# Optimization experiments

Hardware: AMD Instinct MI355X
Metric: run time of the kernel (lower is better)

The kernel has to match this reference:

```python
import jax, jax.numpy as jnp
import numpy as np

M = 16384
C = 128
CLS_W = 8        # cls window size (even)
CLS_C = 64       # cls_depth
REG_W = 3        # reg window size (odd)
CLS_T = 1.0      # cls_temperature
REG_T = 1.0      # reg_temperature
PAD = REG_W // 2
W1 = CLS_W + 2 * PAD  # 10


def setup_inputs() -> dict:
    key = jax.random.key(0)
    k0, k1 = jax.random.split(key)
    feature0 = jax.random.normal(k0, (M, CLS_W * CLS_W, C), dtype=jnp.float32)
    feature1 = jax.random.normal(k1, (M, W1 * W1, C), dtype=jnp.float32)
    return {"feature0": feature0, "feature1": feature1}


def _inner_mask_indices():
    mask = np.zeros((W1, W1), dtype=bool)
    mask[PAD:-PAD, PAD:-PAD] = True
    return jnp.asarray(np.flatnonzero(mask.ravel()))


def reference(feature0, feature1):
    m = feature0.shape[0]
    reg_c = C - CLS_C
    cls_f0, reg_f0 = feature0[..., :CLS_C], feature0[..., CLS_C:]
    cls_f1, reg_f1 = feature1[..., :CLS_C], feature1[..., CLS_C:]

    # ---- cls branch: windowed correlation + dual softmax ----
    cls_f1m = cls_f1[:, _inner_mask_indices(), :]  # [m, cls_w^2, cls_c]
    sim = jnp.einsum('mlc,msc->mls', cls_f0, cls_f1m) / CLS_C / CLS_T
    heatmap = jax.nn.softmax(sim, axis=1) * jax.nn.softmax(sim, axis=2)  # [m, 64, 64]

    ww = CLS_W * CLS_W
    idx = jnp.argmax(heatmap.reshape(m, -1), axis=1)
    idxes0 = (idx // ww)[:, None]
    idxes1 = (idx % ww)[:, None]

    # kornia create_meshgrid(normalized=False): last dim is (x, y)
    ys, xs = jnp.meshgrid(jnp.arange(CLS_W, dtype=jnp.float32),
                          jnp.arange(CLS_W, dtype=jnp.float32), indexing='ij')
    biases = (jnp.stack([xs, ys], axis=-1) - CLS_W // 2 + 0.5).reshape(-1, 2)
    biases0 = biases[idxes0[:, 0]]
    biases1 = biases[idxes1[:, 0]]

    # ---- reg branch: gather window around top cls match, softmax expectation ----
    r = jnp.arange(m)
    rf0 = reg_f0[r, idxes0[:, 0]]                     # [m, reg_c]
    reg_sp = reg_f1.reshape(m, W1, W1, reg_c)         # spatial layout, row-major
    i1 = idxes1[:, 0] // CLS_W                        # top-left row of the reg window
    j1 = idxes1[:, 0] % CLS_W
    rows = i1[:, None] + jnp.arange(REG_W)            # [m, 3]
    cols = j1[:, None] + jnp.arange(REG_W)            # [m, 3]
    patch = reg_sp[r[:, None, None], rows[:, :, None], cols[:, None, :], :]  # [m,3,3,reg_c]
    rf1 = patch.reshape(m, REG_W * REG_W, reg_c)

    sim_r = jnp.einsum('mc,mrc->mr', rf0, rf1) / jnp.sqrt(jnp.float32(reg_c)) / REG_T
    hm_r = jax.nn.softmax(sim_r, axis=1).reshape(m, REG_W, REG_W)

    # kornia spatial_expectation2d with normalized coordinates in [-1, 1]
    lin = jnp.linspace(-1.0, 1.0, REG_W)
    gy, gx = jnp.meshgrid(lin, lin, indexing='ij')
    reg_biases = jnp.stack([jnp.sum(hm_r * gx, axis=(1, 2)),
                            jnp.sum(hm_r * gy, axis=(1, 2))], axis=-1)  # [m, 2]

    return heatmap, idxes0, idxes1, biases0, biases1, reg_biases
```

## Files before the change

kernel.cpp:

```cpp
#include <hip/hip_runtime.h>

__device__ __forceinline__ void gload_lds16(const float* g, float* l) {
  __builtin_amdgcn_global_load_lds(
      (const __attribute__((address_space(1))) unsigned int*)g,
      (__attribute__((address_space(3))) unsigned int*)l, 16, 0, 0);
}

__global__ __launch_bounds__(256, 4) void fm_main_kernel(
    const float* __restrict__ feat0, const float* __restrict__ feat1,
    float* __restrict__ out, int M)
{
  const int t    = threadIdx.x;
  const int lane = t & 63;
  const int wave = t >> 6;

  __shared__ __align__(16) float sA[4096];
  __shared__ __align__(16) float sB[4096];
  __shared__ __align__(16) float colps[4][64];
  __shared__ float redv[4];
  __shared__ int   redi[4];

  const int m = blockIdx.x;
  const float* f0m = feat0 + (size_t)m * 8192;
  const float* f1m = feat1 + (size_t)m * 12800;

  const int pr = lane >> 3;
  const int q  = lane & 7;
#pragma unroll
  for (int h = 0; h < 2; ++h) {
#pragma unroll
    for (int k = 0; k < 2; ++k) {
      const int p0 = wave * 16 + k * 8;
      const int p  = p0 + pr;
      const int gq = q ^ ((p >> 2) & 7);
      gload_lds16(f0m + p * 128 + h * 32 + gq * 4, &sA[h * 2048 + p0 * 32]);
      const int r = ((p >> 3) + 1) * 10 + (p & 7) + 1;
      gload_lds16(f1m + r * 128 + h * 32 + gq * 4, &sB[h * 2048 + p0 * 32]);
    }
  }

  const int st = t & 15, lt = t >> 4;
  const int s4 = st << 2, l4 = lt << 2;
  const int ea = lt & 7, eb = st & 7;

  float acc[4][4] = {};

  asm volatile("s_waitcnt vmcnt(4)" ::: "memory");
  __builtin_amdgcn_s_barrier();
  asm volatile("" ::: "memory");

#pragma unroll
  for (int c8 = 0; c8 < 8; ++c8) {
    float4 a[4], b[4];
    const int qa = (c8 ^ ea) << 2, qb = (c8 ^ eb) << 2;
#pragma unroll
    for (int i = 0; i < 4; ++i) a[i] = *(const float4*)(&sA[(l4 + i) * 32 + qa]);
#pragma unroll
    for (int j = 0; j < 4; ++j) b[j] = *(const float4*)(&sB[(s4 + j) * 32 + qb]);
#pragma unroll
    for (int i = 0; i < 4; ++i)
#pragma unroll
      for (int j = 0; j < 4; ++j)
        acc[i][j] += a[i].x * b[j].x + a[i].y * b[j].y + a[i].z * b[j].z + a[i].w * b[j].w;
  }

  asm volatile("s_waitcnt vmcnt(0)" ::: "memory");
  __builtin_amdgcn_s_barrier();
  asm volatile("" ::: "memory");

#pragma unroll
  for (int c8 = 0; c8 < 8; ++c8) {
    float4 a[4], b[4];
    const int qa = (c8 ^ ea) << 2, qb = (c8 ^ eb) << 2;
#pragma unroll
    for (int i = 0; i < 4; ++i) a[i] = *(const float4*)(&sA[2048 + (l4 + i) * 32 + qa]);
#pragma unroll
    for (int j = 0; j < 4; ++j) b[j] = *(const float4*)(&sB[2048 + (s4 + j) * 32 + qb]);
#pragma unroll
    for (int i = 0; i < 4; ++i)
#pragma unroll
      for (int j = 0; j < 4; ++j)
        acc[i][j] += a[i].x * b[j].x + a[i].y * b[j].y + a[i].z * b[j].z + a[i].w * b[j].w;
  }

  float rinv[4];
#pragma unroll
  for (int i = 0; i < 4; ++i) {
    float rs = 0.0f;
#pragma unroll
    for (int j = 0; j < 4; ++j) { acc[i][j] = __expf(acc[i][j] * 0.015625f); rs += acc[i][j]; }
#pragma unroll
    for (int off = 1; off <= 8; off <<= 1) rs += __shfl_xor(rs, off);
    rinv[i] = 1.0f / rs;
  }
  {
    float cps[4];
#pragma unroll
    for (int j = 0; j < 4; ++j) {
      float cs = acc[0][j] + acc[1][j] + acc[2][j] + acc[3][j];
      cs += __shfl_xor(cs, 16);
      cs += __shfl_xor(cs, 32);
      cps[j] = cs;
    }
    if (lane < 16) *(float4*)(&colps[wave][s4]) = make_float4(cps[0], cps[1], cps[2], cps[3]);
  }
  asm volatile("s_waitcnt lgkmcnt(0)" ::: "memory");
  __builtin_amdgcn_s_barrier();
  asm volatile("" ::: "memory");

  float cinv[4];
  {
    float4 q0 = *(const float4*)(&colps[0][s4]);
    float4 q1 = *(const float4*)(&colps[1][s4]);
    float4 q2 = *(const float4*)(&colps[2][s4]);
    float4 q3 = *(const float4*)(&colps[3][s4]);
    cinv[0] = 1.0f / (q0.x + q1.x + q2.x + q3.x);
    cinv[1] = 1.0f / (q0.y + q1.y + q2.y + q3.y);
    cinv[2] = 1.0f / (q0.z + q1.z + q2.z + q3.z);
    cinv[3] = 1.0f / (q0.w + q1.w + q2.w + q3.w);
  }

  float best = -1.0f; int bidx = 0;
  float* outh = out + (size_t)m * 4096;
#pragma unroll
  for (int i = 0; i < 4; ++i) {
    float ri = rinv[i];
    float4 h;
    h.x = acc[i][0] * acc[i][0] * ri * cinv[0];
    h.y = acc[i][1] * acc[i][1] * ri * cinv[1];
    h.z = acc[i][2] * acc[i][2] * ri * cinv[2];
    h.w = acc[i][3] * acc[i][3] * ri * cinv[3];
    int base = (l4 + i) * 64 + s4;
    *(float4*)(outh + base) = h;
    if (h.x > best) { best = h.x; bidx = base; }
    if (h.y > best) { best = h.y; bidx = base + 1; }
    if (h.z > best) { best = h.z; bidx = base + 2; }
    if (h.w > best) { best = h.w; bidx = base + 3; }
  }
#pragma unroll
  for (int off = 32; off; off >>= 1) {
    float ov = __shfl_xor(best, off);
    int   oi = __shfl_xor(bidx, off);
    if (ov > best || (ov == best && oi < bidx)) { best = ov; bidx = oi; }
  }
  if (lane == 0) { redv[wave] = best; redi[wave] = bidx; }
  asm volatile("s_waitcnt lgkmcnt(0)" ::: "memory");
  __builtin_amdgcn_s_barrier();
  asm volatile("" ::: "memory");

  if (t == 0) {
    float fbv = redv[0]; int fbi = redi[0];
#pragma unroll
    for (int w = 1; w < 4; ++w) {
      float ov = redv[w]; int oi = redi[w];
      if (ov > fbv || (ov == fbv && oi < fbi)) { fbv = ov; fbi = oi; }
    }
    const int i0 = fbi >> 6, i1 = fbi & 63;
    float* oS = out + (size_t)M * 4096;
    oS[m]         = (float)i0;
    oS[M + m]     = (float)i1;
    oS[2 * M + 2 * m + 0] = (float)(i0 & 7) - 3.5f;
    oS[2 * M + 2 * m + 1] = (float)(i0 >> 3) - 3.5f;
    oS[4 * M + 2 * m + 0] = (float)(i1 & 7) - 3.5f;
    oS[4 * M + 2 * m + 1] = (float)(i1 >> 3) - 3.5f;
  }
}

__global__ __launch_bounds__(256, 8) void fm_reg_kernel(
    const float* __restrict__ feat0, const float* __restrict__ feat1,
    float* __restrict__ out, int M)
{
  const int lane = threadIdx.x & 63;
  const int mw   = blockIdx.x * 4 + (threadIdx.x >> 6);
  if (mw >= M) return;

  float* const oS = out + (size_t)M * 4096;
  const int i0 = (int)oS[mw];
  const int i1 = (int)oS[M + mw];

  const float* f0p = feat0 + (size_t)mw * 8192;
  const float* f1p = feat1 + (size_t)mw * 12800;

  const float rf0 = f0p[i0 * 128 + 64 + lane];
  const int r0 = i1 >> 3, c0 = i1 & 7;

  float p[9];
#pragma unroll
  for (int a = 0; a < 3; ++a)
#pragma unroll
    for (int b = 0; b < 3; ++b)
      p[a * 3 + b] = f1p[((r0 + a) * 10 + (c0 + b)) * 128 + 64 + lane] * rf0;

#pragma unroll
  for (int r = 0; r < 9; ++r)
#pragma unroll
    for (int off = 32; off; off >>= 1) p[r] += __shfl_xor(p[r], off);

  if (lane == 0) {
    float mx = p[0];
#pragma unroll
    for (int r = 1; r < 9; ++r) mx = fmaxf(mx, p[r]);
    float e[9], ssum = 0.0f;
#pragma unroll
    for (int r = 0; r < 9; ++r) { e[r] = __expf((p[r] - mx) * 0.125f); ssum += e[r]; }
    float inv = 1.0f / ssum, bx = 0.0f, by = 0.0f;
#pragma unroll
    for (int r = 0; r < 9; ++r) {
      float w = e[r] * inv;
      bx += w * (float)((r % 3) - 1);
      by += w * (float)((r / 3) - 1);
    }
    oS[6 * M + 2 * mw + 0] = bx;
    oS[6 * M + 2 * mw + 1] = by;
  }
}

extern "C" void kernel_launch(void* const* d_in, const int* in_sizes, int n_in,
                              void* d_out, int out_size, void* d_ws, size_t ws_size,
                              hipStream_t stream) {
  const float* f0 = (const float*)d_in[0];
  const float* f1 = (const float*)d_in[1];
  float* out = (float*)d_out;
  int M = in_sizes[0] / 8192;
  fm_main_kernel<<<dim3(M), dim3(256), 0, stream>>>(f0, f1, out, M);
  fm_reg_kernel<<<dim3((M + 3) / 4), dim3(256), 0, stream>>>(f0, f1, out, M);
}
```

Baseline: 238.5 us.

## Use 512-thread blocks with 2x4 per-thread tiles in main correlation kernel

Doubles the workgroup size of the main kernel to 512 threads (8 waves) and shrinks each thread's output tile from 4x4 to 2x4. Each wave now issues half as many async global-to-LDS loads, and the column-sum and argmax reductions extend to 8 waves. The goal is more resident waves per CU to hide memory latency, since LDS usage per block is unchanged. In exchange, the ratio of LDS reads to FMAs rises and reductions carry more overhead.

```diff
diff --git a/kernel.cpp b/kernel.cpp
--- a/kernel.cpp
+++ b/kernel.cpp
@@ -6,7 +6,7 @@
       (__attribute__((address_space(3))) unsigned int*)l, 16, 0, 0);
 }
 
-__global__ __launch_bounds__(256, 4) void fm_main_kernel(
+__global__ __launch_bounds__(512, 8) void fm_main_kernel(
     const float* __restrict__ feat0, const float* __restrict__ feat1,
     float* __restrict__ out, int M)
 {
@@ -16,52 +16,50 @@
 
   __shared__ __align__(16) float sA[4096];
   __shared__ __align__(16) float sB[4096];
-  __shared__ __align__(16) float colps[4][64];
-  __shared__ float redv[4];
-  __shared__ int   redi[4];
+  __shared__ __align__(16) float colps[8][64];
+  __shared__ float redv[8];
+  __shared__ int   redi[8];
 
   const int m = blockIdx.x;
   const float* f0m = feat0 + (size_t)m * 8192;
   const float* f1m = feat1 + (size_t)m * 12800;
 
-  const int pr = lane >> 3;
-  const int q  = lane & 7;
-#pragma unroll
-  for (int h = 0; h < 2; ++h) {
-#pragma unroll
-    for (int k = 0; k < 2; ++k) {
-      const int p0 = wave * 16 + k * 8;
-      const int p  = p0 + pr;
-      const int gq = q ^ ((p >> 2) & 7);
-      gload_lds16(f0m + p * 128 + h * 32 + gq * 4, &sA[h * 2048 + p0 * 32]);
-      const int r = ((p >> 3) + 1) * 10 + (p & 7) + 1;
-      gload_lds16(f1m + r * 128 + h * 32 + gq * 4, &sB[h * 2048 + p0 * 32]);
+  {
+    const int pr = lane >> 3;
+    const int q  = lane & 7;
+    const int p  = wave * 8 + pr;
+    const int gq = q ^ ((p >> 2) & 7);
+    const int r  = ((p >> 3) + 1) * 10 + (p & 7) + 1;
+#pragma unroll
+    for (int h = 0; h < 2; ++h) {
+      gload_lds16(f0m + p * 128 + h * 32 + gq * 4, &sA[h * 2048 + wave * 256]);
+      gload_lds16(f1m + r * 128 + h * 32 + gq * 4, &sB[h * 2048 + wave * 256]);
     }
   }
 
   const int st = t & 15, lt = t >> 4;
-  const int s4 = st << 2, l4 = lt << 2;
-  const int ea = lt & 7, eb = st & 7;
-
-  float acc[4][4] = {};
-
-  asm volatile("s_waitcnt vmcnt(4)" ::: "memory");
+  const int s4 = st << 2, l2 = lt << 1;
+  const int ea = (lt >> 1) & 7, eb = st & 7;
+
+  float acc[2][4] = {};
+
+  asm volatile("s_waitcnt vmcnt(2)" ::: "memory");
   __builtin_amdgcn_s_barrier();
   asm volatile("" ::: "memory");
 
 #pragma unroll
   for (int c8 = 0; c8 < 8; ++c8) {
-    float4 a[4], b[4];
     const int qa = (c8 ^ ea) << 2, qb = (c8 ^ eb) << 2;
-#pragma unroll
-    for (int i = 0; i < 4; ++i) a[i] = *(const float4*)(&sA[(l4 + i) * 32 + qa]);
+    float4 a0 = *(const float4*)(&sA[(l2 + 0) * 32 + qa]);
+    float4 a1 = *(const float4*)(&sA[(l2 + 1) * 32 + qa]);
+    float4 b[4];
 #pragma unroll
     for (int j = 0; j < 4; ++j) b[j] = *(const float4*)(&sB[(s4 + j) * 32 + qb]);
 #pragma unroll
-    for (int i = 0; i < 4; ++i)
-#pragma unroll
-      for (int j = 0; j < 4; ++j)
-        acc[i][j] += a[i].x * b[j].x + a[i].y * b[j].y + a[i].z * b[j].z + a[i].w * b[j].w;
+    for (int j = 0; j < 4; ++j) {
+      acc[0][j] += a0.x * b[j].x + a0.y * b[j].y + a0.z * b[j].z + a0.w * b[j].w;
+      acc[1][j] += a1.x * b[j].x + a1.y * b[j].y + a1.z * b[j].z + a1.w * b[j].w;
+    }
   }
 
   asm volatile("s_waitcnt vmcnt(0)" ::: "memory");
@@ -70,22 +68,22 @@
 
 #pragma unroll
   for (int c8 = 0; c8 < 8; ++c8) {
-    float4 a[4], b[4];
     const int qa = (c8 ^ ea) << 2, qb = (c8 ^ eb) << 2;
-#pragma unroll
-    for (int i = 0; i < 4; ++i) a[i] = *(const float4*)(&sA[2048 + (l4 + i) * 32 + qa]);
+    float4 a0 = *(const float4*)(&sA[2048 + (l2 + 0) * 32 + qa]);
+    float4 a1 = *(const float4*)(&sA[2048 + (l2 + 1) * 32 + qa]);
+    float4 b[4];
 #pragma unroll
     for (int j = 0; j < 4; ++j) b[j] = *(const float4*)(&sB[2048 + (s4 + j) * 32 + qb]);
 #pragma unroll
-    for (int i = 0; i < 4; ++i)
-#pragma unroll
-      for (int j = 0; j < 4; ++j)
-        acc[i][j] += a[i].x * b[j].x + a[i].y * b[j].y + a[i].z * b[j].z + a[i].w * b[j].w;
-  }
-
-  float rinv[4];
-#pragma unroll
-  for (int i = 0; i < 4; ++i) {
+    for (int j = 0; j < 4; ++j) {
+      acc[0][j] += a0.x * b[j].x + a0.y * b[j].y + a0.z * b[j].z + a0.w * b[j].w;
+      acc[1][j] += a1.x * b[j].x + a1.y * b[j].y + a1.z * b[j].z + a1.w * b[j].w;
+    }
+  }
+
+  float rinv[2];
+#pragma unroll
+  for (int i = 0; i < 2; ++i) {
     float rs = 0.0f;
 #pragma unroll
     for (int j = 0; j < 4; ++j) { acc[i][j] = __expf(acc[i][j] * 0.015625f); rs += acc[i][j]; }
@@ -97,7 +95,7 @@
     float cps[4];
 #pragma unroll
     for (int j = 0; j < 4; ++j) {
-      float cs = acc[0][j] + acc[1][j] + acc[2][j] + acc[3][j];
+      float cs = acc[0][j] + acc[1][j];
       cs += __shfl_xor(cs, 16);
       cs += __shfl_xor(cs, 32);
       cps[j] = cs;
@@ -110,27 +108,26 @@
 
   float cinv[4];
   {
-    float4 q0 = *(const float4*)(&colps[0][s4]);
-    float4 q1 = *(const float4*)(&colps[1][s4]);
-    float4 q2 = *(const float4*)(&colps[2][s4]);
-    float4 q3 = *(const float4*)(&colps[3][s4]);
-    cinv[0] = 1.0f / (q0.x + q1.x + q2.x + q3.x);
-    cinv[1] = 1.0f / (q0.y + q1.y + q2.y + q3.y);
-    cinv[2] = 1.0f / (q0.z + q1.z + q2.z + q3.z);
-    cinv[3] = 1.0f / (q0.w + q1.w + q2.w + q3.w);
+    float c0 = 0.0f, c1 = 0.0f, c2 = 0.0f, c3 = 0.0f;
+#pragma unroll
+    for (int w = 0; w < 8; ++w) {
+      float4 qv = *(const float4*)(&colps[w][s4]);
+      c0 += qv.x; c1 += qv.y; c2 += qv.z; c3 += qv.w;
+    }
+    cinv[0] = 1.0f / c0; cinv[1] = 1.0f / c1; cinv[2] = 1.0f / c2; cinv[3] = 1.0f / c3;
   }
 
   float best = -1.0f; int bidx = 0;
   float* outh = out + (size_t)m * 4096;
 #pragma unroll
-  for (int i = 0; i < 4; ++i) {
+  for (int i = 0; i < 2; ++i) {
     float ri = rinv[i];
     float4 h;
     h.x = acc[i][0] * acc[i][0] * ri * cinv[0];
     h.y = acc[i][1] * acc[i][1] * ri * cinv[1];
     h.z = acc[i][2] * acc[i][2] * ri * cinv[2];
     h.w = acc[i][3] * acc[i][3] * ri * cinv[3];
-    int base = (l4 + i) * 64 + s4;
+    int base = (l2 + i) * 64 + s4;
     *(float4*)(outh + base) = h;
     if (h.x > best) { best = h.x; bidx = base; }
     if (h.y > best) { best = h.y; bidx = base + 1; }
@@ -151,7 +148,7 @@
   if (t == 0) {
     float fbv = redv[0]; int fbi = redi[0];
 #pragma unroll
-    for (int w = 1; w < 4; ++w) {
+    for (int w = 1; w < 8; ++w) {
       float ov = redv[w]; int oi = redi[w];
       if (ov > fbv || (ov == fbv && oi < fbi)) { fbv = ov; fbi = oi; }
     }
@@ -222,6 +219,6 @@
   const float* f1 = (const float*)d_in[1];
   float* out = (float*)d_out;
   int M = in_sizes[0] / 8192;
-  fm_main_kernel<<<dim3(M), dim3(256), 0, stream>>>(f0, f1, out, M);
+  fm_main_kernel<<<dim3(M), dim3(512), 0, stream>>>(f0, f1, out, M);
   fm_reg_kernel<<<dim3((M + 3) / 4), dim3(256), 0, stream>>>(f0, f1, out, M);
 }
```

New measurement: 374.7 us. 57.1% more time.

## Load feature0 tile directly from global memory instead of staging in LDS

Applied to the files above, without the earlier changes.

The cls-branch feature0 tile is no longer copied into shared memory. Each thread now reads its four A rows straight from global memory as float4 loads inside the dot-product loop, relying on cache broadcast across the 16 lanes that share a row. Only feature1 is staged in LDS, with a 64-float row layout and a matching XOR swizzle. This halves LDS use and raises the launch-bounds occupancy hint from 4 to 6 blocks, aiming to hide memory latency better. The cost is global-load latency inside the inner loop and the loss of the two-phase wait that overlapped the first half of the compute with the remaining loads.

```diff
diff --git a/kernel.cpp b/kernel.cpp
--- a/kernel.cpp
+++ b/kernel.cpp
@@ -6,7 +6,7 @@
       (__attribute__((address_space(3))) unsigned int*)l, 16, 0, 0);
 }
 
-__global__ __launch_bounds__(256, 4) void fm_main_kernel(
+__global__ __launch_bounds__(256, 6) void fm_main_kernel(
     const float* __restrict__ feat0, const float* __restrict__ feat1,
     float* __restrict__ out, int M)
 {
@@ -14,7 +14,6 @@
   const int lane = t & 63;
   const int wave = t >> 6;
 
-  __shared__ __align__(16) float sA[4096];
   __shared__ __align__(16) float sB[4096];
   __shared__ __align__(16) float colps[4][64];
   __shared__ float redv[4];
@@ -24,58 +23,44 @@
   const float* f0m = feat0 + (size_t)m * 8192;
   const float* f1m = feat1 + (size_t)m * 12800;
 
-  const int pr = lane >> 3;
-  const int q  = lane & 7;
-#pragma unroll
-  for (int h = 0; h < 2; ++h) {
-#pragma unroll
-    for (int k = 0; k < 2; ++k) {
-      const int p0 = wave * 16 + k * 8;
+  {
+    const int pr = lane >> 4;
+    const int q  = lane & 15;
+#pragma unroll
+    for (int k = 0; k < 4; ++k) {
+      const int p0 = wave * 16 + k * 4;
       const int p  = p0 + pr;
-      const int gq = q ^ ((p >> 2) & 7);
-      gload_lds16(f0m + p * 128 + h * 32 + gq * 4, &sA[h * 2048 + p0 * 32]);
-      const int r = ((p >> 3) + 1) * 10 + (p & 7) + 1;
-      gload_lds16(f1m + r * 128 + h * 32 + gq * 4, &sB[h * 2048 + p0 * 32]);
+      const int e  = (p0 >> 2) & 7;
+      const int r  = ((p >> 3) + 1) * 10 + (p & 7) + 1;
+      gload_lds16(f1m + r * 128 + ((q ^ e) << 2), &sB[p0 * 64]);
     }
   }
 
   const int st = t & 15, lt = t >> 4;
   const int s4 = st << 2, l4 = lt << 2;
-  const int ea = lt & 7, eb = st & 7;
+  const int eb = st & 7;
+
+  const float* a0p = f0m + (size_t)(l4 + 0) * 128;
+  const float* a1p = f0m + (size_t)(l4 + 1) * 128;
+  const float* a2p = f0m + (size_t)(l4 + 2) * 128;
+  const float* a3p = f0m + (size_t)(l4 + 3) * 128;
 
   float acc[4][4] = {};
-
-  asm volatile("s_waitcnt vmcnt(4)" ::: "memory");
-  __builtin_amdgcn_s_barrier();
-  asm volatile("" ::: "memory");
-
-#pragma unroll
-  for (int c8 = 0; c8 < 8; ++c8) {
-    float4 a[4], b[4];
-    const int qa = (c8 ^ ea) << 2, qb = (c8 ^ eb) << 2;
-#pragma unroll
-    for (int i = 0; i < 4; ++i) a[i] = *(const float4*)(&sA[(l4 + i) * 32 + qa]);
-#pragma unroll
-    for (int j = 0; j < 4; ++j) b[j] = *(const float4*)(&sB[(s4 + j) * 32 + qb]);
-#pragma unroll
-    for (int i = 0; i < 4; ++i)
-#pragma unroll
-      for (int j = 0; j < 4; ++j)
-        acc[i][j] += a[i].x * b[j].x + a[i].y * b[j].y + a[i].z * b[j].z + a[i].w * b[j].w;
-  }
 
   asm volatile("s_waitcnt vmcnt(0)" ::: "memory");
   __builtin_amdgcn_s_barrier();
   asm volatile("" ::: "memory");
 
 #pragma unroll
-  for (int c8 = 0; c8 < 8; ++c8) {
+  for (int c8 = 0; c8 < 16; ++c8) {
     float4 a[4], b[4];
-    const int qa = (c8 ^ ea) << 2, qb = (c8 ^ eb) << 2;
-#pragma unroll
-    for (int i = 0; i < 4; ++i) a[i] = *(const float4*)(&sA[2048 + (l4 + i) * 32 + qa]);
-#pragma unroll
-    for (int j = 0; j < 4; ++j) b[j] = *(const float4*)(&sB[2048 + (s4 + j) * 32 + qb]);
+    a[0] = *(const float4*)(a0p + c8 * 4);
+    a[1] = *(const float4*)(a1p + c8 * 4);
+    a[2] = *(const float4*)(a2p + c8 * 4);
+    a[3] = *(const float4*)(a3p + c8 * 4);
+    const int qb = (c8 ^ eb) << 2;
+#pragma unroll
+    for (int j = 0; j < 4; ++j) b[j] = *(const float4*)(&sB[(s4 + j) * 64 + qb]);
 #pragma unroll
     for (int i = 0; i < 4; ++i)
 #pragma unroll
```

Result: slower. 744.1 us (+212.0%).
